# Optimization experiments

Hardware: AMD Instinct MI355X
Metric: run time of the kernel (lower is better)

The kernel has to match this reference:

```python
import jax, jax.numpy as jnp
import numpy as np

N_NODES = 100000
HIDDEN = 128
N_ARCS = 1000000


def setup_inputs() -> dict:
    key = jax.random.key(0)
    k1, k2, k3, k4 = jax.random.split(key, 4)
    z = jax.random.normal(k1, (N_NODES, HIDDEN), dtype=jnp.float32)
    pot_arcs = jax.random.randint(k2, (N_ARCS, 2), 0, N_NODES, dtype=jnp.int64)
    # nn.Linear(2H, H): weight [H, 2H], bias [H]
    W1 = jax.random.normal(k3, (HIDDEN, 2 * HIDDEN), dtype=jnp.float32) * (1.0 / np.sqrt(2 * HIDDEN))
    b1 = jnp.zeros((HIDDEN,), dtype=jnp.float32)
    # nn.Linear(H, 1): weight [1, H], bias [1]
    W2 = jax.random.normal(k4, (1, HIDDEN), dtype=jnp.float32) * (1.0 / np.sqrt(HIDDEN))
    b2 = jnp.zeros((1,), dtype=jnp.float32)
    return {"z": z, "pot_arcs": pot_arcs, "W1": W1, "b1": b1, "W2": W2, "b2": b2}


def reference(z, pot_arcs, W1, b1, W2, b2):
    # Gather endpoint embeddings and concat: [E, 2H]
    h = jnp.concatenate([z[pot_arcs[:, 0]], z[pot_arcs[:, 1]]], axis=-1)
    h = jax.nn.relu(h @ W1.T + b1)        # [E, H]
    out = h @ W2.T + b2                   # [E, 1]
    return out.reshape(-1)                # [E]
```

## Files before the change

### kernel.cpp

```cpp
#include <hip/hip_runtime.h>
#include <hip/hip_bf16.h>

#define N_NODES 100000
#define NODES_PAD 100096
#define N_ARCS 1000000

typedef __attribute__((ext_vector_type(8))) short bf16x8;
typedef __attribute__((ext_vector_type(4))) float f32x4;

__device__ __forceinline__ unsigned pk2(float lo, float hi) {
    __hip_bfloat162 b = __float22bfloat162_rn(make_float2(lo, hi));
    union { __hip_bfloat162 b; unsigned u; } c; c.b = b; return c.u;
}

__device__ __forceinline__ uint4 pack8(const float4 a, const float4 b) {
    uint4 r;
    r.x = pk2(a.x, a.y);
    r.y = pk2(a.z, a.w);
    r.z = pk2(b.x, b.y);
    r.w = pk2(b.z, b.w);
    return r;
}

__global__ __launch_bounds__(256) void gemm_uv_q(const float* __restrict__ z,
                                                 const float* __restrict__ W1,
                                                 const float* __restrict__ b1,
                                                 unsigned char* __restrict__ UVq,
                                                 float* __restrict__ scl) {
    __shared__ unsigned short As[64 * 128];
    __shared__ unsigned short Bs[128 * 128];
    const int tid = threadIdx.x;
    const int y = blockIdx.y;
    const int c0 = y * 128;

    #pragma unroll
    for (int it = 0; it < 8; it++) {
        int i = tid + it * 256;
        int row = i >> 4, g = i & 15;
        const float4* s = (const float4*)(W1 + (long)row * 256 + c0 + g * 8);
        ((uint4*)Bs)[row * 16 + (g ^ (row & 15))] = pack8(s[0], s[1]);
    }

    const int lane = tid & 63;
    const int wave = tid >> 6;
    const int l16 = lane & 15;
    const int quad = lane >> 4;

    float bias[8];
    #pragma unroll
    for (int nt = 0; nt < 8; nt++)
        bias[nt] = (y == 0) ? b1[nt * 16 + l16] : 0.0f;

    float* sclh = scl + (long)y * NODES_PAD;

    for (int m0 = blockIdx.x * 64; m0 < N_NODES; m0 += gridDim.x * 64) {
        #pragma unroll
        for (int it = 0; it < 4; it++) {
            int i = tid + it * 256;
            int row = i >> 4, g = i & 15;
            int node = m0 + row;
            uint4 p = make_uint4(0u, 0u, 0u, 0u);
            if (node < N_NODES) {
                const float4* s = (const float4*)(z + (long)node * 128 + g * 8);
                p = pack8(s[0], s[1]);
            }
            ((uint4*)As)[row * 16 + (g ^ (row & 15))] = p;
        }
        __syncthreads();

        const int arow = wave * 16 + l16;
        f32x4 acc[8] = {};
        #pragma unroll
        for (int ks = 0; ks < 4; ks++) {
            const int gb = ks * 4 + quad;
            const bf16x8 a = *(const bf16x8*)&As[arow * 128 + ((gb ^ l16) << 3)];
            #pragma unroll
            for (int nt = 0; nt < 8; nt++) {
                const bf16x8 b = *(const bf16x8*)&Bs[(nt * 16 + l16) * 128 + ((gb ^ l16) << 3)];
                acc[nt] = __builtin_amdgcn_mfma_f32_16x16x32_bf16(a, b, acc[nt], 0, 0, 0);
            }
        }

        float m[4] = {0.f, 0.f, 0.f, 0.f};
        #pragma unroll
        for (int nt = 0; nt < 8; nt++)
            #pragma unroll
            for (int r = 0; r < 4; r++) {
                acc[nt][r] += bias[nt];
                m[r] = fmaxf(m[r], fabsf(acc[nt][r]));
            }
        #pragma unroll
        for (int o = 1; o <= 8; o <<= 1)
            #pragma unroll
            for (int r = 0; r < 4; r++)
                m[r] = fmaxf(m[r], __shfl_xor(m[r], o));

        const int rbase = m0 + wave * 16 + quad * 4;
        float inv[4];
        #pragma unroll
        for (int r = 0; r < 4; r++) {
            m[r] = fmaxf(m[r], 1e-30f);
            inv[r] = 127.0f * __builtin_amdgcn_rcpf(m[r]);
        }
        if (l16 == 0)
            *(float4*)(sclh + rbase) = make_float4(m[0] * (1.f / 127.f), m[1] * (1.f / 127.f),
                                                   m[2] * (1.f / 127.f), m[3] * (1.f / 127.f));
        unsigned char* wp = UVq + (long)rbase * 256 + c0 + l16;
        #pragma unroll
        for (int r = 0; r < 4; r++)
            #pragma unroll
            for (int nt = 0; nt < 8; nt++) {
                int qi = __float2int_rn(acc[nt][r] * inv[r]) + 128;
                wp[(long)r * 256 + nt * 16] = (unsigned char)qi;
            }
        __syncthreads();
    }
}

__global__ __launch_bounds__(256) void arc_score(const int4* __restrict__ arcs4,
                                                 const unsigned char* __restrict__ UVq,
                                                 const float* __restrict__ scl,
                                                 const float* __restrict__ W2,
                                                 const float* __restrict__ b2,
                                                 float* __restrict__ out) {
    const int tid = threadIdx.x;
    const int sub = tid & 15;
    const int gq = blockIdx.x * 16 + (tid >> 4);
    const int eb = sub * 8;

    float w2v[8];
    #pragma unroll
    for (int i = 0; i < 8; i++) w2v[i] = W2[eb + i];
    const float b2s = b2[0];
    const float* sclV = scl + NODES_PAD;

    const long stride = (long)gridDim.x * 32;
    for (long a = (long)gq * 2; a < N_ARCS; a += stride) {
        int4 sd = arcs4[a >> 1];
        const uint2 qu0 = *(const uint2*)(UVq + (long)sd.x * 256 + eb);
        const uint2 qv0 = *(const uint2*)(UVq + (long)sd.y * 256 + 128 + eb);
        const uint2 qu1 = *(const uint2*)(UVq + (long)sd.z * 256 + eb);
        const uint2 qv1 = *(const uint2*)(UVq + (long)sd.w * 256 + 128 + eb);
        const float sU0 = scl[sd.x], sV0 = sclV[sd.y];
        const float sU1 = scl[sd.z], sV1 = sclV[sd.w];
        const float r0 = sV0 * __builtin_amdgcn_rcpf(sU0);
        const float r1 = sV1 * __builtin_amdgcn_rcpf(sU1);
        const float C0 = 128.0f * (1.0f + r0);
        const float C1 = 128.0f * (1.0f + r1);

        float p0 = 0.f, p1 = 0.f;
        const unsigned uw0[2] = {qu0.x, qu0.y}, vw0[2] = {qv0.x, qv0.y};
        const unsigned uw1[2] = {qu1.x, qu1.y}, vw1[2] = {qv1.x, qv1.y};
        #pragma unroll
        for (int w = 0; w < 2; w++) {
            #pragma unroll
            for (int i = 0; i < 4; i++) {
                float gu0 = (float)((uw0[w] >> (8 * i)) & 0xffu);
                float gv0 = (float)((vw0[w] >> (8 * i)) & 0xffu);
                float h0 = fmaf(gv0, r0, gu0 - C0);
                p0 = fmaf(fmaxf(h0, 0.f), w2v[w * 4 + i], p0);
                float gu1 = (float)((uw1[w] >> (8 * i)) & 0xffu);
                float gv1 = (float)((vw1[w] >> (8 * i)) & 0xffu);
                float h1 = fmaf(gv1, r1, gu1 - C1);
                p1 = fmaf(fmaxf(h1, 0.f), w2v[w * 4 + i], p1);
            }
        }
        #pragma unroll
        for (int o = 8; o >= 1; o >>= 1) {
            p0 += __shfl_xor(p0, o);
            p1 += __shfl_xor(p1, o);
        }
        if (sub == 0) {
            out[a] = fmaf(sU0, p0, b2s);
            out[a + 1] = fmaf(sU1, p1, b2s);
        }
    }
}

extern "C" void kernel_launch(void* const* d_in, const int* in_sizes, int n_in,
                              void* d_out, int out_size, void* d_ws, size_t ws_size,
                              hipStream_t stream) {
    const float* z  = (const float*)d_in[0];
    const int4* arcs4 = (const int4*)d_in[1];
    const float* W1 = (const float*)d_in[2];
    const float* b1 = (const float*)d_in[3];
    const float* W2 = (const float*)d_in[4];
    const float* b2 = (const float*)d_in[5];
    float* out = (float*)d_out;

    unsigned char* UVq = (unsigned char*)d_ws;
    float* scl = (float*)((char*)d_ws + (size_t)NODES_PAD * 256);

    hipLaunchKernelGGL(gemm_uv_q, dim3(384, 2), dim3(256), 0, stream,
                       z, W1, b1, UVq, scl);
    hipLaunchKernelGGL(arc_score, dim3(2048), dim3(256), 0, stream,
                       arcs4, UVq, scl, W2, b2, out);
}
```

Baseline: 160.3 us.

## Interleave quantized layout, widen arc gathers to 16B, and software-pipeline arc loop

The GEMM epilogue now packs 8 quantized bytes per thread into one 8-byte store, using an interleaved column layout, instead of scattering single-byte writes. The arc kernel uses 8 lanes per arc with 16-byte gathers, and W2 is permuted to match the new layout. The relu offset is folded into a max against C with a constant correction via the sum of W2. The arc loop is software-pipelined: the index and gathers for the next iteration are issued before the current one is computed. This hides gather latency and cuts instruction count, at the cost of more registers and a clamped prefetch past the end.

```diff
diff --git a/kernel.cpp b/kernel.cpp
--- a/kernel.cpp
+++ b/kernel.cpp
@@ -105,14 +105,21 @@
         if (l16 == 0)
             *(float4*)(sclh + rbase) = make_float4(m[0] * (1.f / 127.f), m[1] * (1.f / 127.f),
                                                    m[2] * (1.f / 127.f), m[3] * (1.f / 127.f));
-        unsigned char* wp = UVq + (long)rbase * 256 + c0 + l16;
-        #pragma unroll
-        for (int r = 0; r < 4; r++)
-            #pragma unroll
-            for (int nt = 0; nt < 8; nt++) {
-                int qi = __float2int_rn(acc[nt][r] * inv[r]) + 128;
-                wp[(long)r * 256 + nt * 16] = (unsigned char)qi;
-            }
+        #pragma unroll
+        for (int r = 0; r < 4; r++) {
+            unsigned lo = 0, hi = 0;
+            #pragma unroll
+            for (int nt = 0; nt < 4; nt++) {
+                unsigned q = (unsigned)__float2int_rn(fmaf(acc[nt][r], inv[r], 128.f));
+                lo |= (q & 0xffu) << (8 * nt);
+            }
+            #pragma unroll
+            for (int nt = 4; nt < 8; nt++) {
+                unsigned q = (unsigned)__float2int_rn(fmaf(acc[nt][r], inv[r], 128.f));
+                hi |= (q & 0xffu) << (8 * (nt - 4));
+            }
+            *(uint2*)(UVq + (long)(rbase + r) * 256 + c0 + l16 * 8) = make_uint2(lo, hi);
+        }
         __syncthreads();
     }
 }
@@ -124,49 +131,71 @@
                                                  const float* __restrict__ b2,
                                                  float* __restrict__ out) {
     const int tid = threadIdx.x;
-    const int sub = tid & 15;
-    const int gq = blockIdx.x * 16 + (tid >> 4);
-    const int eb = sub * 8;
-
-    float w2v[8];
+    const int sub = tid & 7;
+    const int gq = blockIdx.x * 32 + (tid >> 3);
+    const int eb = sub * 16;
+
+    float w2v[16], w2s = 0.f;
     #pragma unroll
-    for (int i = 0; i < 8; i++) w2v[i] = W2[eb + i];
+    for (int i = 0; i < 16; i++) {
+        int col = ((i & 7) << 4) + (sub << 1) + (i >> 3);
+        w2v[i] = W2[col];
+        w2s += w2v[i];
+    }
     const float b2s = b2[0];
     const float* sclV = scl + NODES_PAD;
 
-    const long stride = (long)gridDim.x * 32;
-    for (long a = (long)gq * 2; a < N_ARCS; a += stride) {
-        int4 sd = arcs4[a >> 1];
-        const uint2 qu0 = *(const uint2*)(UVq + (long)sd.x * 256 + eb);
-        const uint2 qv0 = *(const uint2*)(UVq + (long)sd.y * 256 + 128 + eb);
-        const uint2 qu1 = *(const uint2*)(UVq + (long)sd.z * 256 + eb);
-        const uint2 qv1 = *(const uint2*)(UVq + (long)sd.w * 256 + 128 + eb);
-        const float sU0 = scl[sd.x], sV0 = sclV[sd.y];
-        const float sU1 = scl[sd.z], sV1 = sclV[sd.w];
+    const long stride = (long)gridDim.x * 64;
+    const long limp = (long)(N_ARCS - 2) >> 1;
+
+    long a = (long)gq * 2;
+    int4 i0 = arcs4[a >> 1];
+    uint4 u0 = *(const uint4*)(UVq + (long)i0.x * 256 + eb);
+    uint4 v0 = *(const uint4*)(UVq + (long)i0.y * 256 + 128 + eb);
+    uint4 u1 = *(const uint4*)(UVq + (long)i0.z * 256 + eb);
+    uint4 v1 = *(const uint4*)(UVq + (long)i0.w * 256 + 128 + eb);
+    float sU0 = scl[i0.x], sV0 = sclV[i0.y];
+    float sU1 = scl[i0.z], sV1 = sclV[i0.w];
+    long p1i = (a + stride) >> 1; if (p1i > limp) p1i = limp;
+    int4 i1 = arcs4[p1i];
+
+    while (true) {
+        const long an = a + stride;
+        uint4 nu0 = *(const uint4*)(UVq + (long)i1.x * 256 + eb);
+        uint4 nv0 = *(const uint4*)(UVq + (long)i1.y * 256 + 128 + eb);
+        uint4 nu1 = *(const uint4*)(UVq + (long)i1.z * 256 + eb);
+        uint4 nv1 = *(const uint4*)(UVq + (long)i1.w * 256 + 128 + eb);
+        float nsU0 = scl[i1.x], nsV0 = sclV[i1.y];
+        float nsU1 = scl[i1.z], nsV1 = sclV[i1.w];
+        long p2i = (an + stride) >> 1; if (p2i > limp) p2i = limp;
+        int4 i2 = arcs4[p2i];
+
         const float r0 = sV0 * __builtin_amdgcn_rcpf(sU0);
         const float r1 = sV1 * __builtin_amdgcn_rcpf(sU1);
-        const float C0 = 128.0f * (1.0f + r0);
-        const float C1 = 128.0f * (1.0f + r1);
+        const float C0 = fmaf(128.f, r0, 128.f);
+        const float C1 = fmaf(128.f, r1, 128.f);
 
         float p0 = 0.f, p1 = 0.f;
-        const unsigned uw0[2] = {qu0.x, qu0.y}, vw0[2] = {qv0.x, qv0.y};
-        const unsigned uw1[2] = {qu1.x, qu1.y}, vw1[2] = {qv1.x, qv1.y};
-        #pragma unroll
-        for (int w = 0; w < 2; w++) {
-            #pragma unroll
-            for (int i = 0; i < 4; i++) {
-                float gu0 = (float)((uw0[w] >> (8 * i)) & 0xffu);
-                float gv0 = (float)((vw0[w] >> (8 * i)) & 0xffu);
-                float h0 = fmaf(gv0, r0, gu0 - C0);
-                p0 = fmaf(fmaxf(h0, 0.f), w2v[w * 4 + i], p0);
-                float gu1 = (float)((uw1[w] >> (8 * i)) & 0xffu);
-                float gv1 = (float)((vw1[w] >> (8 * i)) & 0xffu);
-                float h1 = fmaf(gv1, r1, gu1 - C1);
-                p1 = fmaf(fmaxf(h1, 0.f), w2v[w * 4 + i], p1);
-            }
-        }
-        #pragma unroll
-        for (int o = 8; o >= 1; o >>= 1) {
+        const unsigned* uw0 = (const unsigned*)&u0;
+        const unsigned* vw0 = (const unsigned*)&v0;
+        const unsigned* uw1 = (const unsigned*)&u1;
+        const unsigned* vw1 = (const unsigned*)&v1;
+        #pragma unroll
+        for (int w = 0; w < 4; w++) {
+            #pragma unroll
+            for (int j = 0; j < 4; j++) {
+                float gu0 = (float)((uw0[w] >> (8 * j)) & 0xffu);
+                float gv0 = (float)((vw0[w] >> (8 * j)) & 0xffu);
+                p0 = fmaf(fmaxf(fmaf(gv0, r0, gu0), C0), w2v[w * 4 + j], p0);
+                float gu1 = (float)((uw1[w] >> (8 * j)) & 0xffu);
+                float gv1 = (float)((vw1[w] >> (8 * j)) & 0xffu);
+                p1 = fmaf(fmaxf(fmaf(gv1, r1, gu1), C1), w2v[w * 4 + j], p1);
+            }
+        }
+        p0 = fmaf(-C0, w2s, p0);
+        p1 = fmaf(-C1, w2s, p1);
+        #pragma unroll
+        for (int o = 4; o >= 1; o >>= 1) {
             p0 += __shfl_xor(p0, o);
             p1 += __shfl_xor(p1, o);
         }
@@ -174,6 +203,12 @@
             out[a] = fmaf(sU0, p0, b2s);
             out[a + 1] = fmaf(sU1, p1, b2s);
         }
+
+        if (an >= N_ARCS) break;
+        a = an;
+        u0 = nu0; v0 = nv0; u1 = nu1; v1 = nv1;
+        sU0 = nsU0; sV0 = nsV0; sU1 = nsU1; sV1 = nsV1;
+        i1 = i2;
     }
 }
 
```

Result: faster. 145.0 us (-9.5%).
